# Kernel tuning notes

Measured on AMD Instinct MI355X. Metric: run time of the kernel, lower is better.

The kernel has to match this reference:

```python
import math
import jax, jax.numpy as jnp
import numpy as np

N, NFEAT, NHID, NCLASS, NLAYERS = 8192, 500, 128, 40, 4
ALPHA, GAMMA, LAMBDA, MAX_W = 0.1, 0.1, 0.5, 0.05


def _col_stochastic(w):
    # Uniform(0,1) -> clamp to [0, MAX_W] -> column normalize (ColumnStochasticGraphConvolution init)
    w = jnp.clip(w, 0.0, MAX_W)
    return w / jnp.clip(w.sum(axis=0, keepdims=True), 1e-8, None)


def setup_inputs() -> dict:
    key = jax.random.key(0)
    ks = jax.random.split(key, 10)
    x = jax.random.normal(ks[0], (N, NFEAT), dtype=jnp.float32)
    adj = (jax.random.uniform(ks[1], (N, N)) < 0.002).astype(jnp.float32)
    s_in = 1.0 / math.sqrt(NFEAT)
    fc_in_w = jax.random.uniform(ks[2], (NFEAT, NHID), minval=-s_in, maxval=s_in, dtype=jnp.float32)
    fc_in_b = jnp.zeros((NHID,), jnp.float32)
    c = jax.random.normal(ks[3], (NHID,), dtype=jnp.float32)
    s_h = 1.0 / math.sqrt(NHID)
    w_gcnii = jax.random.uniform(ks[4], (NLAYERS, NHID, NHID), minval=-s_h, maxval=s_h, dtype=jnp.float32)
    b_gcnii = jax.random.uniform(ks[5], (NLAYERS, NHID), minval=-s_h, maxval=s_h, dtype=jnp.float32)
    w_lin = jax.vmap(_col_stochastic)(jax.random.uniform(ks[6], (NLAYERS, NHID, NHID), dtype=jnp.float32))
    b_lin = jnp.zeros((NLAYERS, NHID), jnp.float32)
    fc_out_w = jax.random.uniform(ks[7], (NHID, NCLASS), minval=-s_h, maxval=s_h, dtype=jnp.float32)
    fc_out_b = jnp.zeros((NCLASS,), jnp.float32)
    return {"x": x, "adj": adj, "fc_in_w": fc_in_w, "fc_in_b": fc_in_b, "c": c,
            "w_gcnii": w_gcnii, "b_gcnii": b_gcnii, "w_lin": w_lin, "b_lin": b_lin,
            "fc_out_w": fc_out_w, "fc_out_b": fc_out_b}


def _normalize_adj(adj):
    # A_hat = D^{-1/2} (A + I) D^{-1/2}
    a = adj + jnp.eye(adj.shape[0], dtype=adj.dtype)
    deg = a.sum(axis=1)
    dinv = jnp.where(deg > 0, jax.lax.rsqrt(deg), 0.0)
    return dinv[:, None] * a * dinv[None, :]


def reference(x, adj, fc_in_w, fc_in_b, c, w_gcnii, b_gcnii, w_lin, b_lin, fc_out_w, fc_out_b):
    a_hat = _normalize_adj(adj)                      # [N, N]
    h = jax.nn.relu(x @ fc_in_w + fc_in_b)           # [N, nhid]
    h = (1.0 - GAMMA) * h + GAMMA * c[None, :]       # H0 preconditioning with learnable c
    h0 = h
    # dropout is identity in eval mode
    for i in range(NLAYERS):
        beta = math.log(LAMBDA / (i + 1) + 1.0)
        # linear propagation branch: A_hat @ (H W'_i) + b'_i  (column-stochastic W')
        linear_part = a_hat @ (h @ w_lin[i]) + b_lin[i]
        # GCNII branch: sigma(((1-a) A_hat H + a H0)((1-b) I + b W_i)) + b_i
        support = (1.0 - ALPHA) * (a_hat @ h) + ALPHA * h0
        gcnii = jax.nn.relu((1.0 - beta) * support + beta * (support @ w_gcnii[i]) + b_gcnii[i])
        h = linear_part + gcnii
    return h @ fc_out_w + fc_out_b                   # [N, nclass] logits
```

## Files before the change

### kernel.cpp

```cpp
#include <hip/hip_runtime.h>
#include <math.h>

#define NROWS 8192
#define NFEATD 500
#define NHID 128
#define NCLS 40
#define CAP 64
#define FCIN_BLOCKS (NROWS / 8)
#define CSR_BLOCKS  (NROWS / 4)
#define ROWS_PB 8

typedef float f32x4 __attribute__((ext_vector_type(4)));

__global__ __launch_bounds__(256) void k_pre(
    const float* __restrict__ x, const float* __restrict__ w,
    const float* __restrict__ b, const float* __restrict__ c,
    const float* __restrict__ adj,
    float* __restrict__ h, float* __restrict__ h0,
    float* __restrict__ dinv, int* __restrict__ cnts, int* __restrict__ cols)
{
    __shared__ float xs[8][504];
    int tid = threadIdx.x;
    if (blockIdx.x < FCIN_BLOCKS) {
        int col = tid & 127;
        int rg = tid >> 7;
        int r0 = blockIdx.x * 8;
        for (int rr = 0; rr < 8; ++rr)
            for (int k = tid; k < NFEATD; k += 256)
                xs[rr][k] = x[(size_t)(r0 + rr) * NFEATD + k];
        __syncthreads();
        float bias = b[col];
        float acc[4] = {bias, bias, bias, bias};
        for (int k4 = 0; k4 < NFEATD / 4; ++k4) {
            int k = k4 * 4;
            f32x4 a0 = *(const f32x4*)&xs[rg * 4 + 0][k];
            f32x4 a1 = *(const f32x4*)&xs[rg * 4 + 1][k];
            f32x4 a2 = *(const f32x4*)&xs[rg * 4 + 2][k];
            f32x4 a3 = *(const f32x4*)&xs[rg * 4 + 3][k];
            float w0 = w[(k + 0) * NHID + col];
            float w1 = w[(k + 1) * NHID + col];
            float w2 = w[(k + 2) * NHID + col];
            float w3 = w[(k + 3) * NHID + col];
            acc[0] += a0.x * w0 + a0.y * w1 + a0.z * w2 + a0.w * w3;
            acc[1] += a1.x * w0 + a1.y * w1 + a1.z * w2 + a1.w * w3;
            acc[2] += a2.x * w0 + a2.y * w1 + a2.z * w2 + a2.w * w3;
            acc[3] += a3.x * w0 + a3.y * w1 + a3.z * w2 + a3.w * w3;
        }
        float cv = c[col];
#pragma unroll
        for (int rr = 0; rr < 4; ++rr) {
            float hv = 0.9f * fmaxf(acc[rr], 0.0f) + 0.1f * cv;
            size_t o = (size_t)(r0 + rg * 4 + rr) * NHID + col;
            h[o] = hv;
            h0[o] = hv;
        }
    } else {
        int bid = blockIdx.x - FCIN_BLOCKS;
        int r = bid * 4 + (tid >> 6);
        int lane = tid & 63;
        const f32x4* row4 = (const f32x4*)(adj + (size_t)r * NROWS);
        int* mycols = cols + (size_t)r * CAP;
        unsigned long long lt = (1ull << lane) - 1ull;
        int cnt = 0;
        for (int it = 0; it < NROWS / 256; ++it) {
            f32x4 v = __builtin_nontemporal_load(&row4[it * 64 + lane]);
            int base = it * 256 + 4 * lane;
            bool nz; unsigned long long m;
            nz = (v.x != 0.0f); m = __ballot(nz);
            if (nz) { int p = cnt + __popcll(m & lt); mycols[p < CAP ? p : CAP - 1] = base; }
            cnt += __popcll(m);
            nz = (v.y != 0.0f); m = __ballot(nz);
            if (nz) { int p = cnt + __popcll(m & lt); mycols[p < CAP ? p : CAP - 1] = base + 1; }
            cnt += __popcll(m);
            nz = (v.z != 0.0f); m = __ballot(nz);
            if (nz) { int p = cnt + __popcll(m & lt); mycols[p < CAP ? p : CAP - 1] = base + 2; }
            cnt += __popcll(m);
            nz = (v.w != 0.0f); m = __ballot(nz);
            if (nz) { int p = cnt + __popcll(m & lt); mycols[p < CAP ? p : CAP - 1] = base + 3; }
            cnt += __popcll(m);
        }
        if (lane == 0) {
            cnts[r] = cnt < CAP ? cnt : CAP;
            dinv[r] = rsqrtf((float)cnt + 1.0f);
        }
    }
}

__global__ __launch_bounds__(256) void k_scale(
    const float* __restrict__ h, const float* __restrict__ dinv,
    float* __restrict__ ht)
{
    int gid = blockIdx.x * 256 + threadIdx.x;
    float2 v = ((const float2*)h)[gid];
    float d = dinv[gid >> 6];
    ((float2*)ht)[gid] = make_float2(v.x * d, v.y * d);
}

__global__ __launch_bounds__(256) void k_layer(
    const float* __restrict__ ht, const float* __restrict__ h0,
    const float* __restrict__ dinv, const int* __restrict__ cnts,
    const int* __restrict__ cols,
    const float* __restrict__ wlin, const float* __restrict__ blin,
    const float* __restrict__ wg, const float* __restrict__ bg,
    float beta, float* __restrict__ htout,
    const float* __restrict__ fow, const float* __restrict__ fob,
    float* __restrict__ out, int final_layer)
{
    __shared__ float ahs[ROWS_PB][NHID];
    __shared__ float ss[ROWS_PB][NHID];
    int tid = threadIdx.x;
    int lane = tid & 63;
    int wid = tid >> 6;
    int r0 = blockIdx.x * ROWS_PB;
    const float2* ht2 = (const float2*)ht;
    const float2* h02 = (const float2*)h0;

    for (int rr = 2 * wid; rr < 2 * wid + 2; ++rr) {
        int r = r0 + rr;
        int n = cnts[r];
        const int* mc = cols + (size_t)r * CAP;
        float ax = 0.f, ay = 0.f;
        int e = 0;
        for (; e + 4 <= n; e += 4) {
            int j0 = mc[e], j1 = mc[e + 1], j2 = mc[e + 2], j3 = mc[e + 3];
            float2 v0 = ht2[(size_t)j0 * 64 + lane];
            float2 v1 = ht2[(size_t)j1 * 64 + lane];
            float2 v2 = ht2[(size_t)j2 * 64 + lane];
            float2 v3 = ht2[(size_t)j3 * 64 + lane];
            ax += v0.x + v1.x + v2.x + v3.x;
            ay += v0.y + v1.y + v2.y + v3.y;
        }
        for (; e < n; ++e) {
            int j = mc[e];
            float2 v = ht2[(size_t)j * 64 + lane];
            ax += v.x;
            ay += v.y;
        }
        float di = dinv[r];
        float2 ti = ht2[(size_t)r * 64 + lane];
        float gx = di * (ax + ti.x);
        float gy = di * (ay + ti.y);
        float2 h0v = h02[(size_t)r * 64 + lane];
        ((float2*)&ahs[rr][0])[lane] = make_float2(gx, gy);
        ((float2*)&ss[rr][0])[lane] =
            make_float2(0.9f * gx + 0.1f * h0v.x, 0.9f * gy + 0.1f * h0v.y);
    }
    __syncthreads();

    int col = tid & 127;
    int rg = tid >> 7;
    float accl[4] = {0, 0, 0, 0};
    float accg[4] = {0, 0, 0, 0};
    for (int k4 = 0; k4 < NHID / 4; ++k4) {
        int k = 4 * k4;
        f32x4 a0 = *(const f32x4*)&ahs[rg * 4 + 0][k];
        f32x4 a1 = *(const f32x4*)&ahs[rg * 4 + 1][k];
        f32x4 a2 = *(const f32x4*)&ahs[rg * 4 + 2][k];
        f32x4 a3 = *(const f32x4*)&ahs[rg * 4 + 3][k];
        f32x4 s0 = *(const f32x4*)&ss[rg * 4 + 0][k];
        f32x4 s1 = *(const f32x4*)&ss[rg * 4 + 1][k];
        f32x4 s2 = *(const f32x4*)&ss[rg * 4 + 2][k];
        f32x4 s3 = *(const f32x4*)&ss[rg * 4 + 3][k];
        float wl0 = wlin[(k + 0) * NHID + col];
        float wl1 = wlin[(k + 1) * NHID + col];
        float wl2 = wlin[(k + 2) * NHID + col];
        float wl3 = wlin[(k + 3) * NHID + col];
        float wg0 = wg[(k + 0) * NHID + col];
        float wg1 = wg[(k + 1) * NHID + col];
        float wg2 = wg[(k + 2) * NHID + col];
        float wg3 = wg[(k + 3) * NHID + col];
        accl[0] += a0.x * wl0 + a0.y * wl1 + a0.z * wl2 + a0.w * wl3;
        accl[1] += a1.x * wl0 + a1.y * wl1 + a1.z * wl2 + a1.w * wl3;
        accl[2] += a2.x * wl0 + a2.y * wl1 + a2.z * wl2 + a2.w * wl3;
        accl[3] += a3.x * wl0 + a3.y * wl1 + a3.z * wl2 + a3.w * wl3;
        accg[0] += s0.x * wg0 + s0.y * wg1 + s0.z * wg2 + s0.w * wg3;
        accg[1] += s1.x * wg0 + s1.y * wg1 + s1.z * wg2 + s1.w * wg3;
        accg[2] += s2.x * wg0 + s2.y * wg1 + s2.z * wg2 + s2.w * wg3;
        accg[3] += s3.x * wg0 + s3.y * wg1 + s3.z * wg2 + s3.w * wg3;
    }
    float blv = blin[col], bgv = bg[col];
    float omb = 1.0f - beta;
    float o[4];
#pragma unroll
    for (int rr = 0; rr < 4; ++rr) {
        float sv = ss[rg * 4 + rr][col];
        float g = fmaxf(omb * sv + beta * accg[rr] + bgv, 0.0f);
        o[rr] = accl[rr] + blv + g;
    }

    if (!final_layer) {
#pragma unroll
        for (int rr = 0; rr < 4; ++rr) {
            int row = r0 + rg * 4 + rr;
            htout[(size_t)row * NHID + col] = dinv[row] * o[rr];
        }
    } else {
        __syncthreads();
#pragma unroll
        for (int rr = 0; rr < 4; ++rr)
            ahs[rg * 4 + rr][col] = o[rr];
        __syncthreads();
        int rr2 = tid >> 6, c2 = tid & 63;
        if (c2 < NCLS) {
#pragma unroll
            for (int half = 0; half < 2; ++half) {
                int lr = half * 4 + rr2;
                float acc = fob[c2];
                for (int k = 0; k < NHID; ++k)
                    acc += ahs[lr][k] * fow[k * NCLS + c2];
                out[(size_t)(r0 + lr) * NCLS + c2] = acc;
            }
        }
    }
}

extern "C" void kernel_launch(void* const* d_in, const int* in_sizes, int n_in,
                              void* d_out, int out_size, void* d_ws, size_t ws_size,
                              hipStream_t stream) {
    const float* x        = (const float*)d_in[0];
    const float* adj      = (const float*)d_in[1];
    const float* fc_in_w  = (const float*)d_in[2];
    const float* fc_in_b  = (const float*)d_in[3];
    const float* c        = (const float*)d_in[4];
    const float* w_gcnii  = (const float*)d_in[5];
    const float* b_gcnii  = (const float*)d_in[6];
    const float* w_lin    = (const float*)d_in[7];
    const float* b_lin    = (const float*)d_in[8];
    const float* fc_out_w = (const float*)d_in[9];
    const float* fc_out_b = (const float*)d_in[10];
    float* out = (float*)d_out;

    char* ws = (char*)d_ws;
    size_t off = 0;
    auto alloc = [&](size_t bytes) -> void* {
        void* p = ws + off;
        off += (bytes + 255) & ~(size_t)255;
        return p;
    };
    float* dinv = (float*)alloc((size_t)NROWS * 4);
    int*   cnts = (int*)  alloc((size_t)NROWS * 4);
    int*   cols = (int*)  alloc((size_t)NROWS * CAP * 4);
    float* hA   = (float*)alloc((size_t)NROWS * NHID * 4);
    float* h0   = (float*)alloc((size_t)NROWS * NHID * 4);
    float* htA  = (float*)alloc((size_t)NROWS * NHID * 4);
    float* htB  = (float*)alloc((size_t)NROWS * NHID * 4);

    k_pre<<<FCIN_BLOCKS + CSR_BLOCKS, 256, 0, stream>>>(
        x, fc_in_w, fc_in_b, c, adj, hA, h0, dinv, cnts, cols);
    k_scale<<<NROWS * 64 / 256, 256, 0, stream>>>(hA, dinv, htA);

    float* htb[2] = {htA, htB};
    for (int i = 0; i < 4; ++i) {
        float beta = logf(0.5f / (float)(i + 1) + 1.0f);
        k_layer<<<NROWS / ROWS_PB, 256, 0, stream>>>(
            htb[i & 1], h0, dinv, cnts, cols,
            w_lin + (size_t)i * NHID * NHID, b_lin + (size_t)i * NHID,
            w_gcnii + (size_t)i * NHID * NHID, b_gcnii + (size_t)i * NHID,
            beta, htb[(i + 1) & 1],
            fc_out_w, fc_out_b, out, (i == 3) ? 1 : 0);
    }
}
```

Measured before the change: 207.9 us.

## Fuse all stages into one persistent cooperative kernel with grid syncs

```diff
diff --git a/kernel.cpp b/kernel.cpp
--- a/kernel.cpp
+++ b/kernel.cpp
@@ -1,149 +1,168 @@
 #include <hip/hip_runtime.h>
+#include <hip/hip_cooperative_groups.h>
 #include <math.h>
+
+namespace cg = cooperative_groups;
 
 #define NROWS 8192
 #define NFEATD 500
 #define NHID 128
 #define NCLS 40
 #define CAP 64
-#define FCIN_BLOCKS (NROWS / 8)
-#define CSR_BLOCKS  (NROWS / 4)
-#define ROWS_PB 8
+#define FCIN_UNITS (NROWS / 8)
+#define CSR_UNITS  (NROWS / 4)
+#define LAYER_UNITS (NROWS / 8)
+#define SMEM_FLOATS 4032
 
 typedef float f32x4 __attribute__((ext_vector_type(4)));
 
-__global__ __launch_bounds__(256) void k_pre(
+
+__device__ __forceinline__ void d_fcin(
     const float* __restrict__ x, const float* __restrict__ w,
-    const float* __restrict__ b, const float* __restrict__ c,
-    const float* __restrict__ adj,
+    const float* __restrict__ b, const float* __restrict__ cvec,
     float* __restrict__ h, float* __restrict__ h0,
-    float* __restrict__ dinv, int* __restrict__ cnts, int* __restrict__ cols)
-{
-    __shared__ float xs[8][504];
-    int tid = threadIdx.x;
-    if (blockIdx.x < FCIN_BLOCKS) {
-        int col = tid & 127;
-        int rg = tid >> 7;
-        int r0 = blockIdx.x * 8;
-        for (int rr = 0; rr < 8; ++rr)
-            for (int k = tid; k < NFEATD; k += 256)
-                xs[rr][k] = x[(size_t)(r0 + rr) * NFEATD + k];
-        __syncthreads();
-        float bias = b[col];
-        float acc[4] = {bias, bias, bias, bias};
-        for (int k4 = 0; k4 < NFEATD / 4; ++k4) {
-            int k = k4 * 4;
-            f32x4 a0 = *(const f32x4*)&xs[rg * 4 + 0][k];
-            f32x4 a1 = *(const f32x4*)&xs[rg * 4 + 1][k];
-            f32x4 a2 = *(const f32x4*)&xs[rg * 4 + 2][k];
-            f32x4 a3 = *(const f32x4*)&xs[rg * 4 + 3][k];
-            float w0 = w[(k + 0) * NHID + col];
-            float w1 = w[(k + 1) * NHID + col];
-            float w2 = w[(k + 2) * NHID + col];
-            float w3 = w[(k + 3) * NHID + col];
-            acc[0] += a0.x * w0 + a0.y * w1 + a0.z * w2 + a0.w * w3;
-            acc[1] += a1.x * w0 + a1.y * w1 + a1.z * w2 + a1.w * w3;
-            acc[2] += a2.x * w0 + a2.y * w1 + a2.z * w2 + a2.w * w3;
-            acc[3] += a3.x * w0 + a3.y * w1 + a3.z * w2 + a3.w * w3;
-        }
-        float cv = c[col];
-#pragma unroll
-        for (int rr = 0; rr < 4; ++rr) {
-            float hv = 0.9f * fmaxf(acc[rr], 0.0f) + 0.1f * cv;
-            size_t o = (size_t)(r0 + rg * 4 + rr) * NHID + col;
-            h[o] = hv;
-            h0[o] = hv;
-        }
-    } else {
-        int bid = blockIdx.x - FCIN_BLOCKS;
-        int r = bid * 4 + (tid >> 6);
-        int lane = tid & 63;
-        const f32x4* row4 = (const f32x4*)(adj + (size_t)r * NROWS);
-        int* mycols = cols + (size_t)r * CAP;
-        unsigned long long lt = (1ull << lane) - 1ull;
-        int cnt = 0;
-        for (int it = 0; it < NROWS / 256; ++it) {
-            f32x4 v = __builtin_nontemporal_load(&row4[it * 64 + lane]);
-            int base = it * 256 + 4 * lane;
-            bool nz; unsigned long long m;
-            nz = (v.x != 0.0f); m = __ballot(nz);
-            if (nz) { int p = cnt + __popcll(m & lt); mycols[p < CAP ? p : CAP - 1] = base; }
-            cnt += __popcll(m);
-            nz = (v.y != 0.0f); m = __ballot(nz);
-            if (nz) { int p = cnt + __popcll(m & lt); mycols[p < CAP ? p : CAP - 1] = base + 1; }
-            cnt += __popcll(m);
-            nz = (v.z != 0.0f); m = __ballot(nz);
-            if (nz) { int p = cnt + __popcll(m & lt); mycols[p < CAP ? p : CAP - 1] = base + 2; }
-            cnt += __popcll(m);
-            nz = (v.w != 0.0f); m = __ballot(nz);
-            if (nz) { int p = cnt + __popcll(m & lt); mycols[p < CAP ? p : CAP - 1] = base + 3; }
-            cnt += __popcll(m);
-        }
-        if (lane == 0) {
-            cnts[r] = cnt < CAP ? cnt : CAP;
-            dinv[r] = rsqrtf((float)cnt + 1.0f);
-        }
-    }
-}
-
-__global__ __launch_bounds__(256) void k_scale(
-    const float* __restrict__ h, const float* __restrict__ dinv,
-    float* __restrict__ ht)
-{
-    int gid = blockIdx.x * 256 + threadIdx.x;
-    float2 v = ((const float2*)h)[gid];
-    float d = dinv[gid >> 6];
-    ((float2*)ht)[gid] = make_float2(v.x * d, v.y * d);
-}
-
-__global__ __launch_bounds__(256) void k_layer(
-    const float* __restrict__ ht, const float* __restrict__ h0,
+    int r0, int tid, float* smemf)
+{
+    float (*xs)[504] = (float(*)[504])smemf;
+    __syncthreads();
+    for (int rr = 0; rr < 8; ++rr)
+        for (int k = tid; k < NFEATD; k += 256)
+            xs[rr][k] = x[(size_t)(r0 + rr) * NFEATD + k];
+    __syncthreads();
+    int col = tid & 127;
+    int rg = tid >> 7;
+    float bias = b[col];
+    float acc[4] = {bias, bias, bias, bias};
+    for (int k4 = 0; k4 < NFEATD / 4; ++k4) {
+        int k = k4 * 4;
+        f32x4 a0 = *(const f32x4*)&xs[rg * 4 + 0][k];
+        f32x4 a1 = *(const f32x4*)&xs[rg * 4 + 1][k];
+        f32x4 a2 = *(const f32x4*)&xs[rg * 4 + 2][k];
+        f32x4 a3 = *(const f32x4*)&xs[rg * 4 + 3][k];
+        float w0 = w[(k + 0) * NHID + col];
+        float w1 = w[(k + 1) * NHID + col];
+        float w2 = w[(k + 2) * NHID + col];
+        float w3 = w[(k + 3) * NHID + col];
+        acc[0] += a0.x * w0 + a0.y * w1 + a0.z * w2 + a0.w * w3;
+        acc[1] += a1.x * w0 + a1.y * w1 + a1.z * w2 + a1.w * w3;
+        acc[2] += a2.x * w0 + a2.y * w1 + a2.z * w2 + a2.w * w3;
+        acc[3] += a3.x * w0 + a3.y * w1 + a3.z * w2 + a3.w * w3;
+    }
+    float cv = cvec[col];
+#pragma unroll
+    for (int rr = 0; rr < 4; ++rr) {
+        float hv = 0.9f * fmaxf(acc[rr], 0.0f) + 0.1f * cv;
+        size_t o = (size_t)(r0 + rg * 4 + rr) * NHID + col;
+        h[o] = hv;
+        h0[o] = hv;
+    }
+}
+
+__device__ __forceinline__ void d_csr(
+    const float* __restrict__ adj, float* __restrict__ dinv,
+    int* __restrict__ cnts, int* __restrict__ cols, int rbase, int tid)
+{
+    int r = rbase + (tid >> 6);
+    int lane = tid & 63;
+    const f32x4* row4 = (const f32x4*)(adj + (size_t)r * NROWS);
+    int* mycols = cols + (size_t)r * CAP;
+    unsigned long long lt = (1ull << lane) - 1ull;
+    int cnt = 0;
+    for (int it = 0; it < NROWS / 256; ++it) {
+        f32x4 v = __builtin_nontemporal_load(&row4[it * 64 + lane]);
+        int base = it * 256 + 4 * lane;
+        bool nz; unsigned long long m;
+        nz = (v.x != 0.0f); m = __ballot(nz);
+        if (nz) { int p = cnt + __popcll(m & lt); mycols[p < CAP ? p : CAP - 1] = base; }
+        cnt += __popcll(m);
+        nz = (v.y != 0.0f); m = __ballot(nz);
+        if (nz) { int p = cnt + __popcll(m & lt); mycols[p < CAP ? p : CAP - 1] = base + 1; }
+        cnt += __popcll(m);
+        nz = (v.z != 0.0f); m = __ballot(nz);
+        if (nz) { int p = cnt + __popcll(m & lt); mycols[p < CAP ? p : CAP - 1] = base + 2; }
+        cnt += __popcll(m);
+        nz = (v.w != 0.0f); m = __ballot(nz);
+        if (nz) { int p = cnt + __popcll(m & lt); mycols[p < CAP ? p : CAP - 1] = base + 3; }
+        cnt += __popcll(m);
+    }
+    if (lane == 0) {
+        cnts[r] = cnt < CAP ? cnt : CAP;
+        dinv[r] = rsqrtf((float)cnt + 1.0f);
+    }
+}
+
+__device__ __forceinline__ void d_layer(
+    const float* __restrict__ hin, const float* __restrict__ h0,
     const float* __restrict__ dinv, const int* __restrict__ cnts,
     const int* __restrict__ cols,
     const float* __restrict__ wlin, const float* __restrict__ blin,
-    const float* __restrict__ wg, const float* __restrict__ bg,
+    const float* __restrict__ wgm, const float* __restrict__ bg,
     float beta, float* __restrict__ htout,
     const float* __restrict__ fow, const float* __restrict__ fob,
-    float* __restrict__ out, int final_layer)
-{
-    __shared__ float ahs[ROWS_PB][NHID];
-    __shared__ float ss[ROWS_PB][NHID];
-    int tid = threadIdx.x;
+    float* __restrict__ out, int edge_dinv, int final_layer,
+    int r0, int tid, float* smemf)
+{
+    float (*ahs)[NHID] = (float(*)[NHID])smemf;
+    float (*ss)[NHID]  = (float(*)[NHID])(smemf + 8 * NHID);
     int lane = tid & 63;
     int wid = tid >> 6;
-    int r0 = blockIdx.x * ROWS_PB;
-    const float2* ht2 = (const float2*)ht;
+    const float2* h2 = (const float2*)hin;
     const float2* h02 = (const float2*)h0;
 
+    __syncthreads();
     for (int rr = 2 * wid; rr < 2 * wid + 2; ++rr) {
         int r = r0 + rr;
         int n = cnts[r];
         const int* mc = cols + (size_t)r * CAP;
         float ax = 0.f, ay = 0.f;
         int e = 0;
-        for (; e + 4 <= n; e += 4) {
-            int j0 = mc[e], j1 = mc[e + 1], j2 = mc[e + 2], j3 = mc[e + 3];
-            float2 v0 = ht2[(size_t)j0 * 64 + lane];
-            float2 v1 = ht2[(size_t)j1 * 64 + lane];
-            float2 v2 = ht2[(size_t)j2 * 64 + lane];
-            float2 v3 = ht2[(size_t)j3 * 64 + lane];
-            ax += v0.x + v1.x + v2.x + v3.x;
-            ay += v0.y + v1.y + v2.y + v3.y;
-        }
-        for (; e < n; ++e) {
-            int j = mc[e];
-            float2 v = ht2[(size_t)j * 64 + lane];
-            ax += v.x;
-            ay += v.y;
-        }
-        float di = dinv[r];
-        float2 ti = ht2[(size_t)r * 64 + lane];
-        float gx = di * (ax + ti.x);
-        float gy = di * (ay + ti.y);
+        if (edge_dinv) {
+            for (; e + 4 <= n; e += 4) {
+                int j0 = mc[e], j1 = mc[e + 1], j2 = mc[e + 2], j3 = mc[e + 3];
+                float d0 = dinv[j0], d1 = dinv[j1], d2 = dinv[j2], d3 = dinv[j3];
+                float2 v0 = h2[(size_t)j0 * 64 + lane];
+                float2 v1 = h2[(size_t)j1 * 64 + lane];
+                float2 v2 = h2[(size_t)j2 * 64 + lane];
+                float2 v3 = h2[(size_t)j3 * 64 + lane];
+                ax += d0 * v0.x + d1 * v1.x + d2 * v2.x + d3 * v3.x;
+                ay += d0 * v0.y + d1 * v1.y + d2 * v2.y + d3 * v3.y;
+            }
+            for (; e < n; ++e) {
+                int j = mc[e];
+                float dj = dinv[j];
+                float2 v = h2[(size_t)j * 64 + lane];
+                ax += dj * v.x;
+                ay += dj * v.y;
+            }
+            float di = dinv[r];
+            float2 vi = h2[(size_t)r * 64 + lane];
+            ax = di * (ax + di * vi.x);
+            ay = di * (ay + di * vi.y);
+        } else {
+            for (; e + 4 <= n; e += 4) {
+                int j0 = mc[e], j1 = mc[e + 1], j2 = mc[e + 2], j3 = mc[e + 3];
+                float2 v0 = h2[(size_t)j0 * 64 + lane];
+                float2 v1 = h2[(size_t)j1 * 64 + lane];
+                float2 v2 = h2[(size_t)j2 * 64 + lane];
+                float2 v3 = h2[(size_t)j3 * 64 + lane];
+                ax += v0.x + v1.x + v2.x + v3.x;
+                ay += v0.y + v1.y + v2.y + v3.y;
+            }
+            for (; e < n; ++e) {
+                int j = mc[e];
+                float2 v = h2[(size_t)j * 64 + lane];
+                ax += v.x;
+                ay += v.y;
+            }
+            float di = dinv[r];
+            float2 ti = h2[(size_t)r * 64 + lane];
+            ax = di * (ax + ti.x);
+            ay = di * (ay + ti.y);
+        }
         float2 h0v = h02[(size_t)r * 64 + lane];
-        ((float2*)&ahs[rr][0])[lane] = make_float2(gx, gy);
+        ((float2*)&ahs[rr][0])[lane] = make_float2(ax, ay);
         ((float2*)&ss[rr][0])[lane] =
-            make_float2(0.9f * gx + 0.1f * h0v.x, 0.9f * gy + 0.1f * h0v.y);
+            make_float2(0.9f * ax + 0.1f * h0v.x, 0.9f * ay + 0.1f * h0v.y);
     }
     __syncthreads();
 
@@ -165,10 +184,10 @@
         float wl1 = wlin[(k + 1) * NHID + col];
         float wl2 = wlin[(k + 2) * NHID + col];
         float wl3 = wlin[(k + 3) * NHID + col];
-        float wg0 = wg[(k + 0) * NHID + col];
-        float wg1 = wg[(k + 1) * NHID + col];
-        float wg2 = wg[(k + 2) * NHID + col];
-        float wg3 = wg[(k + 3) * NHID + col];
+        float wg0 = wgm[(k + 0) * NHID + col];
+        float wg1 = wgm[(k + 1) * NHID + col];
+        float wg2 = wgm[(k + 2) * NHID + col];
+        float wg3 = wgm[(k + 3) * NHID + col];
         accl[0] += a0.x * wl0 + a0.y * wl1 + a0.z * wl2 + a0.w * wl3;
         accl[1] += a1.x * wl0 + a1.y * wl1 + a1.z * wl2 + a1.w * wl3;
         accl[2] += a2.x * wl0 + a2.y * wl1 + a2.z * wl2 + a2.w * wl3;
@@ -214,6 +233,84 @@
     }
 }
 
+__global__ __launch_bounds__(256, 4) void k_mega(
+    const float* x, const float* adj,
+    const float* fiw, const float* fib, const float* cvec,
+    const float* wg_all, const float* bg_all,
+    const float* wl_all, const float* bl_all,
+    const float* fow, const float* fob,
+    float* out, float* dinv, int* cnts, int* cols,
+    float* hA, float* h0, float* htA, float* htB)
+{
+    cg::grid_group grid = cg::this_grid();
+    __shared__ float smem[SMEM_FLOATS];
+    const int tid = threadIdx.x;
+    const int bid = blockIdx.x;
+    const int G = gridDim.x;
+
+    if (bid & 1) {
+        for (int u = FCIN_UNITS + bid; u < FCIN_UNITS + CSR_UNITS; u += G)
+            d_csr(adj, dinv, cnts, cols, (u - FCIN_UNITS) * 4, tid);
+        for (int u = bid; u < FCIN_UNITS; u += G)
+            d_fcin(x, fiw, fib, cvec, hA, h0, u * 8, tid, smem);
+    } else {
+        for (int u = bid; u < FCIN_UNITS; u += G)
+            d_fcin(x, fiw, fib, cvec, hA, h0, u * 8, tid, smem);
+        for (int u = FCIN_UNITS + bid; u < FCIN_UNITS + CSR_UNITS; u += G)
+            d_csr(adj, dinv, cnts, cols, (u - FCIN_UNITS) * 4, tid);
+    }
+    __threadfence();
+    grid.sync();
+
+    const float* hbufs[5]  = {hA, htA, htB, htA, nullptr};
+    float* obufs[4]        = {htA, htB, htA, nullptr};
+    for (int i = 0; i < 4; ++i) {
+        float beta = logf(0.5f / (float)(i + 1) + 1.0f);
+        const float* wl = wl_all + (size_t)i * NHID * NHID;
+        const float* wg = wg_all + (size_t)i * NHID * NHID;
+        const float* bl = bl_all + (size_t)i * NHID;
+        const float* bg = bg_all + (size_t)i * NHID;
+        for (int u = bid; u < LAYER_UNITS; u += G)
+            d_layer(hbufs[i], h0, dinv, cnts, cols, wl, bl, wg, bg, beta,
+                    obufs[i], fow, fob, out,
+                    (i == 0) ? 1 : 0, (i == 3) ? 1 : 0, u * 8, tid, smem);
+        if (i < 3) {
+            __threadfence();
+            grid.sync();
+        }
+    }
+}
+
+__global__ __launch_bounds__(256) void k_pre(
+    const float* __restrict__ x, const float* __restrict__ w,
+    const float* __restrict__ b, const float* __restrict__ cvec,
+    const float* __restrict__ adj,
+    float* __restrict__ h, float* __restrict__ h0,
+    float* __restrict__ dinv, int* __restrict__ cnts, int* __restrict__ cols)
+{
+    __shared__ float smem[SMEM_FLOATS];
+    if (blockIdx.x < FCIN_UNITS)
+        d_fcin(x, w, b, cvec, h, h0, blockIdx.x * 8, threadIdx.x, smem);
+    else
+        d_csr(adj, dinv, cnts, cols, (blockIdx.x - FCIN_UNITS) * 4, threadIdx.x);
+}
+
+__global__ __launch_bounds__(256) void k_layer(
+    const float* __restrict__ hin, const float* __restrict__ h0,
+    const float* __restrict__ dinv, const int* __restrict__ cnts,
+    const int* __restrict__ cols,
+    const float* __restrict__ wlin, const float* __restrict__ blin,
+    const float* __restrict__ wgm, const float* __restrict__ bg,
+    float beta, float* __restrict__ htout,
+    const float* __restrict__ fow, const float* __restrict__ fob,
+    float* __restrict__ out, int edge_dinv, int final_layer)
+{
+    __shared__ float smem[SMEM_FLOATS];
+    d_layer(hin, h0, dinv, cnts, cols, wlin, blin, wgm, bg, beta, htout,
+            fow, fob, out, edge_dinv, final_layer, blockIdx.x * 8,
+            threadIdx.x, smem);
+}
+
 extern "C" void kernel_launch(void* const* d_in, const int* in_sizes, int n_in,
                               void* d_out, int out_size, void* d_ws, size_t ws_size,
                               hipStream_t stream) {
@@ -221,7 +318,7 @@
     const float* adj      = (const float*)d_in[1];
     const float* fc_in_w  = (const float*)d_in[2];
     const float* fc_in_b  = (const float*)d_in[3];
-    const float* c        = (const float*)d_in[4];
+    const float* cvec     = (const float*)d_in[4];
     const float* w_gcnii  = (const float*)d_in[5];
     const float* b_gcnii  = (const float*)d_in[6];
     const float* w_lin    = (const float*)d_in[7];
@@ -245,18 +342,38 @@
     float* htA  = (float*)alloc((size_t)NROWS * NHID * 4);
     float* htB  = (float*)alloc((size_t)NROWS * NHID * 4);
 
-    k_pre<<<FCIN_BLOCKS + CSR_BLOCKS, 256, 0, stream>>>(
-        x, fc_in_w, fc_in_b, c, adj, hA, h0, dinv, cnts, cols);
-    k_scale<<<NROWS * 64 / 256, 256, 0, stream>>>(hA, dinv, htA);
-
-    float* htb[2] = {htA, htB};
-    for (int i = 0; i < 4; ++i) {
-        float beta = logf(0.5f / (float)(i + 1) + 1.0f);
-        k_layer<<<NROWS / ROWS_PB, 256, 0, stream>>>(
-            htb[i & 1], h0, dinv, cnts, cols,
-            w_lin + (size_t)i * NHID * NHID, b_lin + (size_t)i * NHID,
-            w_gcnii + (size_t)i * NHID * NHID, b_gcnii + (size_t)i * NHID,
-            beta, htb[(i + 1) & 1],
-            fc_out_w, fc_out_b, out, (i == 3) ? 1 : 0);
-    }
-}
+    bool coop_done = false;
+    int occ = 0;
+    hipError_t qe = hipOccupancyMaxActiveBlocksPerMultiprocessor(
+        &occ, (const void*)k_mega, 256, 0);
+    if (qe == hipSuccess && occ > 0) {
+        int G = occ * 256;
+        if (G > 1024) G = 1024;
+        void* args[] = {
+            (void*)&x, (void*)&adj, (void*)&fc_in_w, (void*)&fc_in_b,
+            (void*)&cvec, (void*)&w_gcnii, (void*)&b_gcnii, (void*)&w_lin,
+            (void*)&b_lin, (void*)&fc_out_w, (void*)&fc_out_b,
+            (void*)&out, (void*)&dinv, (void*)&cnts, (void*)&cols,
+            (void*)&hA, (void*)&h0, (void*)&htA, (void*)&htB,
+        };
+        hipError_t le = hipLaunchCooperativeKernel(
+            (const void*)k_mega, dim3(G), dim3(256), args, 0, stream);
+        coop_done = (le == hipSuccess);
+    }
+
+    if (!coop_done) {
+        k_pre<<<FCIN_UNITS + CSR_UNITS, 256, 0, stream>>>(
+            x, fc_in_w, fc_in_b, cvec, adj, hA, h0, dinv, cnts, cols);
+        const float* hbufs[4] = {hA, htA, htB, htA};
+        float* obufs[4] = {htA, htB, htA, nullptr};
+        for (int i = 0; i < 4; ++i) {
+            float beta = logf(0.5f / (float)(i + 1) + 1.0f);
+            k_layer<<<LAYER_UNITS, 256, 0, stream>>>(
+                hbufs[i], h0, dinv, cnts, cols,
+                w_lin + (size_t)i * NHID * NHID, b_lin + (size_t)i * NHID,
+                w_gcnii + (size_t)i * NHID * NHID, b_gcnii + (size_t)i * NHID,
+                beta, obufs[i], fc_out_w, fc_out_b, out,
+                (i == 0) ? 1 : 0, (i == 3) ? 1 : 0);
+        }
+    }
+}
```

After: 764.2 us. +267.5%, slower.
